# Kernel tuning notes

Hardware: AMD Instinct MI355X
Metric: run time of the kernel (lower is better)

## Reference

```python
import jax, jax.numpy as jnp
import numpy as np

NGRAMS = (1, 2, 3, 4)


def _conv1d(x, W, b):
    # x: [B, S, E], W: [D, E, K], b: [D] -> [B, S-K+1, D] (valid conv, torch Conv1d)
    y = jax.lax.conv_general_dilated(
        x.transpose(0, 2, 1), W, window_strides=(1,), padding='VALID',
        dimension_numbers=('NCH', 'OIH', 'NCH'))
    return y.transpose(0, 2, 1) + b


def setup_inputs() -> dict:
    key = jax.random.key(0)
    ks = jax.random.split(key, 9)
    B, S, E, D = 64, 512, 256, 512
    inp = {'features': jax.random.normal(ks[0], (B, S, E), dtype=jnp.float32)}
    for i, n in enumerate(NGRAMS):
        fan_in = E * n
        inp[f'W{n}'] = jax.random.normal(ks[1 + 2 * i], (D, E, n), dtype=jnp.float32) / np.sqrt(fan_in)
        inp[f'b{n}'] = jax.random.normal(ks[2 + 2 * i], (D,), dtype=jnp.float32) * 0.01
    return inp


def reference(features, W1, b1, W2, b2, W3, b3, W4, b4):
    Ws = (W1, W2, W3, W4)
    bs = (b1, b2, b3, b4)
    # n-gram conv branches: branch g has kernel size NGRAMS[g] = g+1, length S - g
    feats = [_conv1d(features, W, b) for W, b in zip(Ws, bs)]
    B, S, E = features.shape
    flen = E  # faithful to original: features_len = features.shape[-1] (the embed dim)
    out = feats[0]  # unigram features, [B, S, D]
    i = jnp.arange(flen)
    add = jnp.zeros((B, flen, out.shape[-1]), out.dtype)
    # Original nested loops: out[:, i] += sum_{g=1}^{maxn-1} sum_{p=max(0,i-g+1)}^{min(i+1,L_g)-1} feats[g][:, p]
    # Computed here with per-branch prefix sums (exclusive) -> windowed sums.
    for g in range(1, max(NGRAMS)):
        y = feats[g]                      # [B, L, D], L = S - g
        L = y.shape[1]
        P = jnp.concatenate([jnp.zeros_like(y[:, :1]), jnp.cumsum(y, axis=1)], axis=1)  # [B, L+1, D]
        hi = jnp.minimum(i + 1, L)
        lo = jnp.minimum(jnp.maximum(0, i - g + 1), L)
        win = P[:, hi] - P[:, lo]         # [B, flen, D]
        add = add + jnp.where((hi > lo)[None, :, None], win, jnp.zeros_like(win))
    return out.at[:, :flen].add(add)
```

## Files before the change

### kernel.cpp

```cpp
#include <hip/hip_runtime.h>
#include <hip/hip_bf16.h>

#define EDIM 256
#define SDIM 512
#define BDIM 64
#define DDIM 512
#define SPAD 514

#define OFF_XP    0u
#define OFF_GINTB 16842752u
#define OFF_W1B   18415616u
#define OFF_CORR  18677760u
#define OFF_BI    18939904u

#define CVT_BLOCKS  4112
#define WB_BASE     4112
#define CORR_BASE   4624
#define PREP_BLOCKS 8720

typedef __attribute__((ext_vector_type(8))) __bf16 bf16x8;
typedef __attribute__((ext_vector_type(4))) float  f32x4;
typedef __attribute__((ext_vector_type(8))) unsigned short ushort8v;

__device__ __forceinline__ unsigned short f2bf(float f) {
    unsigned int u = __float_as_uint(f);
    u = (u + 0x7fffu + ((u >> 16) & 1u)) >> 16;
    return (unsigned short)u;
}

__global__ __launch_bounds__(256) void prep_all(
    const float* __restrict__ X,
    const float* __restrict__ W1, const float* __restrict__ b1,
    const float* __restrict__ W2, const float* __restrict__ b2,
    const float* __restrict__ W3, const float* __restrict__ b3,
    const float* __restrict__ W4, const float* __restrict__ b4,
    char* __restrict__ wsb)
{
    const int tid = threadIdx.x;

    if (blockIdx.x < CVT_BLOCKS) {
        unsigned short* Xp = (unsigned short*)(wsb + OFF_XP);
        const int i   = blockIdx.x * 256 + tid;
        const int row = i >> 5;
        const int q   = i & 31;
        const int b   = row / SPAD;
        const int j   = row - b * SPAD;
        ushort8v v;
        if (j < 2) {
            v = (ushort8v)0;
        } else {
            const float* src = X + ((size_t)(b * SDIM + j - 2)) * EDIM + q * 8;
            const float4 f0 = *(const float4*)(src);
            const float4 f1 = *(const float4*)(src + 4);
            v[0] = f2bf(f0.x); v[1] = f2bf(f0.y); v[2] = f2bf(f0.z); v[3] = f2bf(f0.w);
            v[4] = f2bf(f1.x); v[5] = f2bf(f1.y); v[6] = f2bf(f1.z); v[7] = f2bf(f1.w);
        }
        *(ushort8v*)(Xp + (size_t)row * EDIM + q * 8) = v;
        return;
    }

    if (blockIdx.x < CORR_BASE) {
        const int d = blockIdx.x - WB_BASE;
        const int e = tid;
        const int de = d * EDIM + e;

        const float w1  = W1[de];
        const float w20 = W2[de * 2 + 0], w21 = W2[de * 2 + 1];
        const float w30 = W3[de * 3 + 0], w31 = W3[de * 3 + 1], w32 = W3[de * 3 + 2];
        const float w40 = W4[de * 4 + 0], w41 = W4[de * 4 + 1], w42 = W4[de * 4 + 2], w43 = W4[de * 4 + 3];

        unsigned short* Gi = (unsigned short*)(wsb + OFF_GINTB) + (size_t)d * 1536;
        Gi[0 * EDIM + e] = f2bf(w40);
        Gi[1 * EDIM + e] = f2bf(w30 + w40 + w41);
        Gi[2 * EDIM + e] = f2bf(w1 + w20 + w30 + w31 + w40 + w41 + w42);
        Gi[3 * EDIM + e] = f2bf(w21 + w31 + w32 + w41 + w42 + w43);
        Gi[4 * EDIM + e] = f2bf(w32 + w42 + w43);
        Gi[5 * EDIM + e] = f2bf(w43);

        ((unsigned short*)(wsb + OFF_W1B))[de] = f2bf(w1);

        if (e == 0)
            ((float*)(wsb + OFF_BI))[d] = b1[d] + b2[d] + 2.0f * b3[d] + 3.0f * b4[d];
        return;
    }

    {
        __shared__ float cls[16];
        const int cb = blockIdx.x - CORR_BASE;
        const int d  = cb >> 3;
        const int bq = (cb & 7) * 8;
        const int e  = tid;

        if (tid < 16) cls[tid] = 0.f;

        const float w31 = W3[(size_t)d * 768 + 3 * e + 1];
        const float w32 = W3[(size_t)d * 768 + 3 * e + 2];
        const float4 w4v = *(const float4*)(W4 + (size_t)d * 1024 + 4 * e);
        const float w41 = w4v.y, w42 = w4v.z, w43 = w4v.w;

        const float c00 = w31 + w41 + w42;
        const float c01 = w32 + w42 + w43;
        const float c02 = w43;
        __syncthreads();

#pragma unroll
        for (int bi = 0; bi < 8; ++bi) {
            const float* xr = X + (size_t)(bq + bi) * (SDIM * EDIM) + e;
            const float x0 = xr[0], x1 = xr[EDIM], x2 = xr[2 * EDIM];
            float a0 = c00 * x0 + c01 * x1 + c02 * x2;
            float a1 = w41 * x0 + w42 * x1 + w43 * x2;
#pragma unroll
            for (int off = 32; off >= 1; off >>= 1) {
                a0 += __shfl_xor(a0, off, 64);
                a1 += __shfl_xor(a1, off, 64);
            }
            if ((tid & 63) == 0) {
                atomicAdd(&cls[bi * 2 + 0], a0);
                atomicAdd(&cls[bi * 2 + 1], a1);
            }
        }
        __syncthreads();

        if (tid < 16) {
            const int s = tid & 1;
            const float bc = s ? b4[d] : (b3[d] + 2.f * b4[d]);
            ((float*)(wsb + OFF_CORR))[(size_t)d * 128 + bq * 2 + tid] = -cls[tid] - bc;
        }
    }
}

__global__ __launch_bounds__(256) void mega(
    const unsigned short* __restrict__ Xp,
    const char* __restrict__ wsb,
    const float* __restrict__ b1,
    float* __restrict__ out)
{
    __shared__ __align__(16) char smem[16384];
    const int id  = blockIdx.x;
    const int tid = threadIdx.x;

    const bool is_tail = id >= 512;
    const int  idx  = is_tail ? id - 512 : id;
    const int  row0 = (idx & 127) * 128;
    const int  col0 = (idx >> 7) * 128;
    const int  K     = is_tail ? 256 : 1536;
    const int  s_lo  = is_tail ? 256 : 0;
    const int  aoff  = is_tail ? 2 : 0;
    const unsigned short* Gbf = is_tail ? (const unsigned short*)(wsb + OFF_W1B)
                                        : (const unsigned short*)(wsb + OFF_GINTB);
    const float* bias = is_tail ? b1 : (const float*)(wsb + OFF_BI);

    unsigned short* Alds = (unsigned short*)smem;
    unsigned short* Blds = (unsigned short*)(smem + 8192);

    const int w = tid >> 6;
    const int l = tid & 63;

    const int sub = l >> 2;
    const int kb  = (l & 3) * 16;

    const int ra0 = row0 + 32 * w + sub;
    const int ra1 = ra0 + 16;
    const int ba0 = ra0 >> 8, sa0 = ra0 & 255;
    const int ba1 = ra1 >> 8, sa1 = ra1 & 255;
    const char* ga0 = (const char*)(Xp + ((size_t)(ba0 * SPAD + s_lo + sa0 + aoff)) * EDIM) + kb;
    const char* ga1 = (const char*)(Xp + ((size_t)(ba1 * SPAD + s_lo + sa1 + aoff)) * EDIM) + kb;
    const char* gb0 = (const char*)(Gbf + (size_t)(col0 + 32 * w + sub) * K) + kb;
    const char* gb1 = (const char*)(Gbf + (size_t)(col0 + 32 * w + 16 + sub) * K) + kb;

    unsigned short* la0 = Alds + (32 * w) * 32;
    unsigned short* la1 = Alds + (32 * w + 16) * 32;
    unsigned short* lb0 = Blds + (32 * w) * 32;
    unsigned short* lb1 = Blds + (32 * w + 16) * 32;

    const int wr  = (w >> 1) * 64;
    const int wc  = (w & 1) * 64;
    const int fm  = l & 15;
    const int fkb = (l >> 4) * 16;

    f32x4 acc[4][4] = {};
    const char* Ab = (const char*)Alds;
    const char* Bb = (const char*)Blds;

    const int nk = K >> 5;
    for (int kt = 0; kt < nk; ++kt) {
        __syncthreads();
        __builtin_amdgcn_global_load_lds((const __attribute__((address_space(1))) void*)ga0,
                                         (__attribute__((address_space(3))) void*)la0, 16, 0, 0);
        __builtin_amdgcn_global_load_lds((const __attribute__((address_space(1))) void*)ga1,
                                         (__attribute__((address_space(3))) void*)la1, 16, 0, 0);
        __builtin_amdgcn_global_load_lds((const __attribute__((address_space(1))) void*)gb0,
                                         (__attribute__((address_space(3))) void*)lb0, 16, 0, 0);
        __builtin_amdgcn_global_load_lds((const __attribute__((address_space(1))) void*)gb1,
                                         (__attribute__((address_space(3))) void*)lb1, 16, 0, 0);
        ga0 += 64; ga1 += 64; gb0 += 64; gb1 += 64;
        __syncthreads();

        bf16x8 af[4], bfr[4];
#pragma unroll
        for (int t = 0; t < 4; ++t) {
            af[t]  = *(const bf16x8*)(Ab + (wr + t * 16 + fm) * 64 + fkb);
            bfr[t] = *(const bf16x8*)(Bb + (wc + t * 16 + fm) * 64 + fkb);
        }
#pragma unroll
        for (int i = 0; i < 4; ++i)
#pragma unroll
            for (int j = 0; j < 4; ++j)
                acc[i][j] = __builtin_amdgcn_mfma_f32_16x16x32_bf16(af[i], bfr[j], acc[i][j], 0, 0, 0);
    }

    const float* corr = (const float*)(wsb + OFF_CORR);
    const int ocol = col0 + wc + fm;
    const int rq   = (l >> 4) * 4;
    float bv[4];
#pragma unroll
    for (int j = 0; j < 4; ++j) bv[j] = bias[ocol + j * 16];

#pragma unroll
    for (int i = 0; i < 4; ++i) {
#pragma unroll
        for (int r = 0; r < 4; ++r) {
            const int rr  = row0 + wr + i * 16 + rq + r;
            const int ssl = rr & 255;
            const int bb  = rr >> 8;
            const int ss  = s_lo + ssl;
            float* op = out + ((size_t)(bb * SDIM + ss)) * DDIM + ocol;
            if (!is_tail && ssl < 2) {
                const float* cp = corr + (size_t)ocol * 128 + bb * 2 + ssl;
#pragma unroll
                for (int j = 0; j < 4; ++j)
                    op[j * 16] = acc[i][j][r] + bv[j] + cp[(size_t)j * 16 * 128];
            } else {
#pragma unroll
                for (int j = 0; j < 4; ++j)
                    op[j * 16] = acc[i][j][r] + bv[j];
            }
        }
    }
}

extern "C" void kernel_launch(void* const* d_in, const int* in_sizes, int n_in,
                              void* d_out, int out_size, void* d_ws, size_t ws_size,
                              hipStream_t stream)
{
    const float* X  = (const float*)d_in[0];
    const float* W1 = (const float*)d_in[1];
    const float* b1 = (const float*)d_in[2];
    const float* W2 = (const float*)d_in[3];
    const float* b2 = (const float*)d_in[4];
    const float* W3 = (const float*)d_in[5];
    const float* b3 = (const float*)d_in[6];
    const float* W4 = (const float*)d_in[7];
    const float* b4 = (const float*)d_in[8];
    float* out = (float*)d_out;
    char*  wsb = (char*)d_ws;

    prep_all<<<dim3(PREP_BLOCKS), dim3(256), 0, stream>>>(X, W1, b1, W2, b2, W3, b3, W4, b4, wsb);

    mega<<<dim3(1024), dim3(256), 0, stream>>>(
        (const unsigned short*)(wsb + OFF_XP), wsb, b1, out);
}
```

Baseline: 164.1 us.

## Triple-buffer LDS tiles with async prefetch and XOR-swizzle layout in GEMM

Replaces the single-buffer load/sync/compute loop with a three-stage LDS ring. Tiles are prefetched two k-steps ahead using global_load_lds, and manual vmcnt waits plus a raw barrier stand in for the double __syncthreads. The 16-byte chunk positions in each LDS row are also XOR-swizzled to reduce bank conflicts on the fragment reads. Shared memory use triples to 48KB, which may reduce occupancy, and the hand-written waitcnt counts must match the number of loads in flight.

```diff
diff --git a/kernel.cpp b/kernel.cpp
--- a/kernel.cpp
+++ b/kernel.cpp
@@ -129,13 +129,17 @@
     }
 }
 
+#define GLL(src, dst) \
+    __builtin_amdgcn_global_load_lds((const __attribute__((address_space(1))) void*)(src), \
+                                     (__attribute__((address_space(3))) void*)(dst), 16, 0, 0)
+
 __global__ __launch_bounds__(256) void mega(
     const unsigned short* __restrict__ Xp,
     const char* __restrict__ wsb,
     const float* __restrict__ b1,
     float* __restrict__ out)
 {
-    __shared__ __align__(16) char smem[16384];
+    __shared__ __align__(16) char smem[49152];
     const int id  = blockIdx.x;
     const int tid = threadIdx.x;
 
@@ -150,64 +154,79 @@
                                         : (const unsigned short*)(wsb + OFF_GINTB);
     const float* bias = is_tail ? b1 : (const float*)(wsb + OFF_BI);
 
-    unsigned short* Alds = (unsigned short*)smem;
-    unsigned short* Blds = (unsigned short*)(smem + 8192);
-
     const int w = tid >> 6;
     const int l = tid & 63;
 
     const int sub = l >> 2;
-    const int kb  = (l & 3) * 16;
+    const int swz = (((l & 3) ^ ((sub >> 1) & 3)) * 16);
 
     const int ra0 = row0 + 32 * w + sub;
     const int ra1 = ra0 + 16;
     const int ba0 = ra0 >> 8, sa0 = ra0 & 255;
     const int ba1 = ra1 >> 8, sa1 = ra1 & 255;
-    const char* ga0 = (const char*)(Xp + ((size_t)(ba0 * SPAD + s_lo + sa0 + aoff)) * EDIM) + kb;
-    const char* ga1 = (const char*)(Xp + ((size_t)(ba1 * SPAD + s_lo + sa1 + aoff)) * EDIM) + kb;
-    const char* gb0 = (const char*)(Gbf + (size_t)(col0 + 32 * w + sub) * K) + kb;
-    const char* gb1 = (const char*)(Gbf + (size_t)(col0 + 32 * w + 16 + sub) * K) + kb;
-
-    unsigned short* la0 = Alds + (32 * w) * 32;
-    unsigned short* la1 = Alds + (32 * w + 16) * 32;
-    unsigned short* lb0 = Blds + (32 * w) * 32;
-    unsigned short* lb1 = Blds + (32 * w + 16) * 32;
+    const char* ga0 = (const char*)(Xp + ((size_t)(ba0 * SPAD + s_lo + sa0 + aoff)) * EDIM) + swz;
+    const char* ga1 = (const char*)(Xp + ((size_t)(ba1 * SPAD + s_lo + sa1 + aoff)) * EDIM) + swz;
+    const char* gb0 = (const char*)(Gbf + (size_t)(col0 + 32 * w + sub) * K) + swz;
+    const char* gb1 = (const char*)(Gbf + (size_t)(col0 + 32 * w + 16 + sub) * K) + swz;
+
+    const int oA0 = (32 * w) * 64;
+    const int oA1 = (32 * w + 16) * 64;
+    const int oB0 = 8192 + (32 * w) * 64;
+    const int oB1 = 8192 + (32 * w + 16) * 64;
+
+    char* Buf0 = smem;
+    char* Buf1 = smem + 16384;
+    char* Buf2 = smem + 32768;
 
     const int wr  = (w >> 1) * 64;
     const int wc  = (w & 1) * 64;
     const int fm  = l & 15;
-    const int fkb = (l >> 4) * 16;
+    const int rslot = (((l >> 4) ^ ((fm >> 1) & 3)) * 16);
+    const int rdA = (wr + fm) * 64 + rslot;
+    const int rdB = 8192 + (wc + fm) * 64 + rslot;
 
     f32x4 acc[4][4] = {};
-    const char* Ab = (const char*)Alds;
-    const char* Bb = (const char*)Blds;
-
-    const int nk = K >> 5;
-    for (int kt = 0; kt < nk; ++kt) {
-        __syncthreads();
-        __builtin_amdgcn_global_load_lds((const __attribute__((address_space(1))) void*)ga0,
-                                         (__attribute__((address_space(3))) void*)la0, 16, 0, 0);
-        __builtin_amdgcn_global_load_lds((const __attribute__((address_space(1))) void*)ga1,
-                                         (__attribute__((address_space(3))) void*)la1, 16, 0, 0);
-        __builtin_amdgcn_global_load_lds((const __attribute__((address_space(1))) void*)gb0,
-                                         (__attribute__((address_space(3))) void*)lb0, 16, 0, 0);
-        __builtin_amdgcn_global_load_lds((const __attribute__((address_space(1))) void*)gb1,
-                                         (__attribute__((address_space(3))) void*)lb1, 16, 0, 0);
+
+    auto STAGE = [&](char* buf) {
+        GLL(ga0, buf + oA0);
+        GLL(ga1, buf + oA1);
+        GLL(gb0, buf + oB0);
+        GLL(gb1, buf + oB1);
         ga0 += 64; ga1 += 64; gb0 += 64; gb1 += 64;
-        __syncthreads();
-
+    };
+
+    auto COMPUTE = [&](const char* buf) {
         bf16x8 af[4], bfr[4];
 #pragma unroll
         for (int t = 0; t < 4; ++t) {
-            af[t]  = *(const bf16x8*)(Ab + (wr + t * 16 + fm) * 64 + fkb);
-            bfr[t] = *(const bf16x8*)(Bb + (wc + t * 16 + fm) * 64 + fkb);
+            af[t]  = *(const bf16x8*)(buf + rdA + t * 1024);
+            bfr[t] = *(const bf16x8*)(buf + rdB + t * 1024);
         }
 #pragma unroll
         for (int i = 0; i < 4; ++i)
 #pragma unroll
             for (int j = 0; j < 4; ++j)
                 acc[i][j] = __builtin_amdgcn_mfma_f32_16x16x32_bf16(af[i], bfr[j], acc[i][j], 0, 0, 0);
-    }
+    };
+
+    const int nk = K >> 5;
+
+    STAGE(Buf0);
+    STAGE(Buf1);
+    char* p0 = Buf0;
+    char* p1 = Buf1;
+    char* p2 = Buf2;
+
+    for (int kt = 0; kt < nk - 1; ++kt) {
+        asm volatile("s_waitcnt vmcnt(4) lgkmcnt(0)" ::: "memory");
+        __builtin_amdgcn_s_barrier();
+        if (kt < nk - 2) STAGE(p2);
+        COMPUTE(p0);
+        char* t0 = p0; p0 = p1; p1 = p2; p2 = t0;
+    }
+    asm volatile("s_waitcnt vmcnt(0) lgkmcnt(0)" ::: "memory");
+    __builtin_amdgcn_s_barrier();
+    COMPUTE(p0);
 
     const float* corr = (const float*)(wsb + OFF_CORR);
     const int ocol = col0 + wc + fm;
```

Result: no change. 161.1 us (-1.8%).
